# Kernel optimization log

Hardware: AMD Instinct MI355X
Metric: run time of the kernel (lower is better)

The kernel has to match this reference:

```python
import jax, jax.numpy as jnp
import numpy as np

NUM_HEADS = 8
GROUPS = 32  # min(32, 512 // 4)
EPS = 1e-5


def group_norm(y, gamma, beta):
    B, C, L = y.shape
    yg = y.reshape(B, GROUPS, -1)  # [B, G, (C//G)*L]
    mu = yg.mean(-1, keepdims=True)
    var = yg.var(-1, keepdims=True)
    yn = ((yg - mu) * jax.lax.rsqrt(var + EPS)).reshape(B, C, L)
    return yn * gamma[:, None] + beta[:, None]


def setup_inputs() -> dict:
    key = jax.random.key(0)
    ks = jax.random.split(key, 5)
    B, C, L = 4, 512, 2048
    return {
        "x": jax.random.normal(ks[0], (B, C, L), dtype=jnp.float32),
        "Wqkv": jax.random.normal(ks[1], (3 * C, C), dtype=jnp.float32) * (C ** -0.5),
        "bqkv": jax.random.normal(ks[2], (3 * C,), dtype=jnp.float32) * 0.01,
        "Wproj": jax.random.normal(ks[3], (C, C), dtype=jnp.float32) * (C ** -0.5),
        "bproj": jax.random.normal(ks[4], (C,), dtype=jnp.float32) * 0.01,
        "gamma": jnp.ones((C,), dtype=jnp.float32),
        "beta": jnp.zeros((C,), dtype=jnp.float32),
    }


def reference(x, Wqkv, bqkv, Wproj, bproj, gamma, beta):
    B, C, L = x.shape
    H = NUM_HEADS
    D = C // H
    # 1x1 Conv1d == channel-mixing matmul
    qkv = jnp.einsum('oc,bcl->bol', Wqkv, x) + bqkv[:, None]  # [B, 3C, L]
    qkv = qkv.reshape(B, 3, H, D, L)
    q, k, v = qkv[:, 0], qkv[:, 1], qkv[:, 2]
    q = jnp.clip(q, -10.0, 10.0)
    k = jnp.clip(k, -10.0, 10.0)
    v = jnp.clip(v, -10.0, 10.0)
    scale = D ** -0.5
    attn = jnp.einsum('bhdi,bhdj->bhij', q, k) * scale  # [B, H, L, L]
    attn = jnp.clip(attn, -10.0, 10.0)
    attn = jax.nn.softmax(attn, axis=-1)
    # NaN fallback: replace whole attn with identity if any NaN (matches torch branch)
    has_nan = jnp.isnan(attn).any()
    attn = jnp.where(has_nan, jnp.eye(L, dtype=x.dtype), attn)
    out = jnp.einsum('bhij,bhdj->bhdi', attn, v)  # [B, H, D, L]
    out = out.reshape(B, C, L)
    out = jnp.einsum('oc,bcl->bol', Wproj, out) + bproj[:, None]
    return group_norm(out + x, gamma, beta)
```

## Files before the change

### kernel.cpp

```cpp
#include <hip/hip_runtime.h>
#include <cstddef>

#define B_ 4
#define C_ 512
#define L_ 2048

typedef __attribute__((ext_vector_type(8))) short  short8;
typedef __attribute__((ext_vector_type(4))) float  f32x4;
typedef __attribute__((ext_vector_type(4))) unsigned short us4;

#define AS1 __attribute__((address_space(1)))
#define AS3 __attribute__((address_space(3)))

__device__ __forceinline__ float clip10(float v){ return fminf(fmaxf(v,-10.0f),10.0f); }

__device__ __forceinline__ unsigned short f2bf(float f){
  union { float f; unsigned u; } v; v.f = f;
  unsigned r = v.u + 0x7fffu + ((v.u >> 16) & 1u);
  return (unsigned short)(r >> 16);
}
__device__ __forceinline__ unsigned pk_tr(float lo, float hi){
  return __builtin_amdgcn_perm(__float_as_uint(hi), __float_as_uint(lo), 0x07060302u);
}
__device__ __forceinline__ float bf2f(unsigned short u){
  return __uint_as_float(((unsigned)u)<<16);
}
__device__ __forceinline__ void gl16(const void* g, void* l){
  __builtin_amdgcn_global_load_lds((const AS1 unsigned*)g, (AS3 unsigned*)l, 16, 0, 0);
}

__global__ __launch_bounds__(256) void prep_k(
    const float* __restrict__ x, const float* __restrict__ Wq,
    const float* __restrict__ Wp, unsigned short* __restrict__ xT,
    unsigned short* __restrict__ Wqb, unsigned short* __restrict__ Wpb)
{
  const int blk = blockIdx.x;
  const int t = threadIdx.x;
  if (blk < 4096){
    __shared__ float tile[32][33];
    const int b = blk>>10, rem = blk&1023;
    const int c0 = (rem>>6)*32, l0 = (rem&63)*32;
    const int cr = t>>3, lc = (t&7)*4;
    const float4 v = *(const float4*)(x + ((size_t)b*C_ + c0+cr)*L_ + l0 + lc);
    tile[cr][lc]=v.x; tile[cr][lc+1]=v.y; tile[cr][lc+2]=v.z; tile[cr][lc+3]=v.w;
    __syncthreads();
    const int lr = t>>3, cc = (t&7)*4;
    const us4 o = { f2bf(tile[cc][lr]), f2bf(tile[cc+1][lr]),
                    f2bf(tile[cc+2][lr]), f2bf(tile[cc+3][lr]) };
    *(us4*)(xT + ((size_t)b*L_ + l0+lr)*C_ + c0 + cc) = o;
  } else {
    const int i = (blk-4096)*256 + t;
    const int NQ = 1536*512/4;
    const float* src; unsigned short* dst; int j;
    if (i < NQ){ src = Wq; dst = Wqb; j = i; }
    else       { src = Wp; dst = Wpb; j = i - NQ; }
    const float4 v = *(const float4*)(src + (size_t)j*4);
    const us4 o = { f2bf(v.x), f2bf(v.y), f2bf(v.z), f2bf(v.w) };
    *(us4*)(dst + (size_t)j*4) = o;
  }
}

template<int MODE>
__global__ __launch_bounds__(256) void mfma_gemm(
    const unsigned short* __restrict__ Wb, const unsigned short* __restrict__ Bin,
    const float* __restrict__ bias,
    unsigned short* __restrict__ qT, unsigned short* __restrict__ kT,
    unsigned short* __restrict__ vN, float* __restrict__ yout)
{
  __shared__ unsigned short SA[128*64];
  __shared__ unsigned short SB[128*64];
  const int t = threadIdx.x;
  const int b = blockIdx.z;
  const int mb = blockIdx.y, n0 = blockIdx.x*128, m0 = mb*128;
  const int lane = t&63, w = t>>6, wm = w>>1, wn = w&1;
  const int n = lane&15, q4 = lane>>4;

  f32x4 acc[4][4];
#pragma unroll
  for (int i=0;i<4;i++)
#pragma unroll
    for (int j=0;j<4;j++) acc[i][j] = (f32x4){0.f,0.f,0.f,0.f};

  const unsigned short* Arow = Wb + (size_t)m0*512;
  const unsigned short* Brow = Bin + ((size_t)b*L_ + n0)*512;

  for (int kt=0; kt<8; kt++){
    const int k0 = kt*64;
    __syncthreads();
#pragma unroll
    for (int i=0;i<4;i++){
      const int ch = t + 256*i;
      const int row = ch>>3, lc = (ch&7) ^ (row&7);
      gl16(Arow + (size_t)row*512 + k0 + lc*8, &SA[ch*8]);
      gl16(Brow + (size_t)row*512 + k0 + lc*8, &SB[ch*8]);
    }
    __syncthreads();
#pragma unroll
    for (int kk=0;kk<2;kk++){
      short8 aF[4], bF[4];
      const int pc = ((kk*4+q4) ^ (n&7))*8;
#pragma unroll
      for (int mt=0;mt<4;mt++) aF[mt] = *(const short8*)&SA[(wm*64+mt*16+n)*64 + pc];
#pragma unroll
      for (int nt=0;nt<4;nt++) bF[nt] = *(const short8*)&SB[(wn*64+nt*16+n)*64 + pc];
#pragma unroll
      for (int mt=0;mt<4;mt++)
#pragma unroll
        for (int nt=0;nt<4;nt++)
          acc[mt][nt] = __builtin_amdgcn_mfma_f32_16x16x32_bf16(aF[mt], bF[nt], acc[mt][nt], 0,0,0);
    }
  }

  const float QS = 0.180336880f;
#pragma unroll
  for (int mt=0;mt<4;mt++){
    const int obase = m0 + wm*64 + mt*16 + q4*4;
    const float b0=bias[obase], b1=bias[obase+1], b2=bias[obase+2], b3=bias[obase+3];
#pragma unroll
    for (int nt=0;nt<4;nt++){
      const int l = n0 + wn*64 + nt*16 + n;
      float r0=acc[mt][nt][0]+b0, r1=acc[mt][nt][1]+b1,
            r2=acc[mt][nt][2]+b2, r3=acc[mt][nt][3]+b3;
      if (MODE==0){
        r0=clip10(r0); r1=clip10(r1); r2=clip10(r2); r3=clip10(r3);
        const int typ = mb>>2;
        const int oin = obase - typ*512;
        if (typ < 2){
          if (typ==0){ r0*=QS; r1*=QS; r2*=QS; r3*=QS; }
          unsigned short* dst = (typ==0) ? qT : kT;
          const us4 o = { f2bf(r0), f2bf(r1), f2bf(r2), f2bf(r3) };
          *(us4*)&dst[((size_t)b*L_ + l)*512 + oin] = o;
        } else {
          unsigned short* dst = vN + ((size_t)b*512 + oin)*L_ + l;
          dst[0]=f2bf(r0); dst[(size_t)L_]=f2bf(r1);
          dst[(size_t)2*L_]=f2bf(r2); dst[(size_t)3*L_]=f2bf(r3);
        }
      } else {
        float* dst = yout + ((size_t)b*512 + obase)*L_ + l;
        dst[0]=r0; dst[(size_t)L_]=r1; dst[(size_t)2*L_]=r2; dst[(size_t)3*L_]=r3;
      }
    }
  }
}

#define PP 72

__global__ __launch_bounds__(256,4) void attn_v8(
    const unsigned short* __restrict__ qT, const unsigned short* __restrict__ kT,
    const unsigned short* __restrict__ vN,
    unsigned short* __restrict__ Opart, float* __restrict__ den)
{
  __shared__ unsigned short s_k[64*64];
  __shared__ unsigned short s_v[64*64];
  __shared__ unsigned short s_p[128*PP];
  const int t  = threadIdx.x;
  const int io = blockIdx.x>>1, half = blockIdx.x&1;
  const int i0 = io*128;
  const int h  = blockIdx.y, b = blockIdx.z;
  const int lane = t&63, w = t>>6, n = lane&15, q4 = lane>>4;
  const int idx = ((b*8+h)*16+io)*2 + half;

  const unsigned short* kb0 = kT + (size_t)b*L_*512 + h*64;
  const unsigned short* vb  = vN + ((size_t)b*512 + h*64)*L_;

  short8 qf[2][2];
#pragma unroll
  for (int mt=0; mt<2; mt++)
#pragma unroll
    for (int kk=0; kk<2; kk++)
      qf[mt][kk] = *(const short8*)(qT + ((size_t)b*L_ + i0 + w*32 + mt*16 + n)*512
                                       + h*64 + kk*32 + q4*8);

  f32x4 oacc[2][4];
  float dacc[2];
#pragma unroll
  for (int mt=0;mt<2;mt++){ dacc[mt]=0.f;
#pragma unroll
    for (int dt=0;dt<4;dt++) oacc[mt][dt]=(f32x4){0.f,0.f,0.f,0.f}; }

  const float LIM = 14.4269504089f;
  const int jbeg = half*1024, jend = jbeg+1024;

  for (int j0=jbeg; j0<jend; j0+=64){
    __syncthreads();
#pragma unroll
    for (int i=0;i<2;i++){
      const int ch = t + 256*i, row = ch>>3, lc = (ch&7)^(row&7);
      gl16(kb0 + (size_t)(j0+row)*512 + lc*8, &s_k[ch*8]);
      gl16(vb  + (size_t)row*L_ + j0 + lc*8,  &s_v[ch*8]);
    }
    __syncthreads();

    f32x4 sacc[2][4];
#pragma unroll
    for (int mt=0;mt<2;mt++)
#pragma unroll
      for (int jt=0;jt<4;jt++) sacc[mt][jt]=(f32x4){0.f,0.f,0.f,0.f};
#pragma unroll
    for (int kk=0;kk<2;kk++){
      const int pc = ((kk*4+q4) ^ (n&7))*8;
      short8 aK[4];
#pragma unroll
      for (int jt=0;jt<4;jt++) aK[jt] = *(const short8*)&s_k[(jt*16+n)*64 + pc];
#pragma unroll
      for (int mt=0;mt<2;mt++)
#pragma unroll
        for (int jt=0;jt<4;jt++)
          sacc[mt][jt] = __builtin_amdgcn_mfma_f32_16x16x32_bf16(aK[jt], qf[mt][kk], sacc[mt][jt], 0,0,0);
    }

#pragma unroll
    for (int mt=0;mt<2;mt++)
#pragma unroll
      for (int jt=0;jt<4;jt++){
        const float e0 = __builtin_amdgcn_exp2f(__builtin_amdgcn_fmed3f(sacc[mt][jt][0],-LIM,LIM));
        const float e1 = __builtin_amdgcn_exp2f(__builtin_amdgcn_fmed3f(sacc[mt][jt][1],-LIM,LIM));
        const float e2 = __builtin_amdgcn_exp2f(__builtin_amdgcn_fmed3f(sacc[mt][jt][2],-LIM,LIM));
        const float e3 = __builtin_amdgcn_exp2f(__builtin_amdgcn_fmed3f(sacc[mt][jt][3],-LIM,LIM));
        dacc[mt] += (e0+e1)+(e2+e3);
        const unsigned long long pv =
            (unsigned long long)pk_tr(e0,e1) | ((unsigned long long)pk_tr(e2,e3)<<32);
        *(unsigned long long*)&s_p[(w*32 + mt*16 + n)*PP + jt*16 + q4*4] = pv;
      }

#pragma unroll
    for (int kk=0;kk<2;kk++){
      const int pcv = ((kk*4+q4) ^ (n&7))*8;
      short8 bV[4], pA[2];
#pragma unroll
      for (int dt=0;dt<4;dt++) bV[dt] = *(const short8*)&s_v[(dt*16+n)*64 + pcv];
#pragma unroll
      for (int mt=0;mt<2;mt++)
        pA[mt] = *(const short8*)&s_p[(w*32 + mt*16 + n)*PP + kk*32 + q4*8];
#pragma unroll
      for (int mt=0;mt<2;mt++)
#pragma unroll
        for (int dt=0;dt<4;dt++)
          oacc[mt][dt] = __builtin_amdgcn_mfma_f32_16x16x32_bf16(pA[mt], bV[kk==0?dt:dt], oacc[mt][dt], 0,0,0);
    }
  }

#pragma unroll
  for (int mt=0;mt<2;mt++){
    float d = dacc[mt];
    d += __shfl_xor(d, 16);
    d += __shfl_xor(d, 32);
    if (q4 == 0) den[(size_t)idx*128 + w*32 + mt*16 + n] = d;
  }

#pragma unroll
  for (int mt=0;mt<2;mt++)
#pragma unroll
    for (int dt=0;dt<4;dt++)
#pragma unroll
      for (int r=0;r<4;r++)
        Opart[(size_t)idx*8192 + (w*32 + mt*16 + q4*4 + r)*64 + dt*16 + n]
            = f2bf(oacc[mt][dt][r]);
}

__global__ __launch_bounds__(256) void attn_combine(
    const unsigned short* __restrict__ Opart, const float* __restrict__ den,
    unsigned short* __restrict__ attnT)
{
  __shared__ float s_inv[128];
  const int io = blockIdx.x, h = blockIdx.y, b = blockIdx.z;
  const int t = threadIdx.x;
  const int base = ((b*8+h)*16+io)*2;
  if (t < 128)
    s_inv[t] = 1.0f/(den[(size_t)base*128 + t] + den[(size_t)(base+1)*128 + t]);
  __syncthreads();
  const unsigned short* O0 = Opart + (size_t)base*8192;
  const unsigned short* O1 = O0 + 8192;
#pragma unroll
  for (int it=0; it<8; it++){
    const int chunk = it*256 + t;
    const int i = chunk>>4, c4 = (chunk&15)*4;
    const us4 a = *(const us4*)&O0[i*64 + c4];
    const us4 c = *(const us4*)&O1[i*64 + c4];
    const float inv = s_inv[i];
    const us4 o = { f2bf((bf2f(a[0])+bf2f(c[0]))*inv),
                    f2bf((bf2f(a[1])+bf2f(c[1]))*inv),
                    f2bf((bf2f(a[2])+bf2f(c[2]))*inv),
                    f2bf((bf2f(a[3])+bf2f(c[3]))*inv) };
    *(us4*)&attnT[((size_t)b*L_ + io*128 + i)*512 + h*64 + c4] = o;
  }
}

__global__ __launch_bounds__(256) void gn_stats(
    const float* __restrict__ y, const float* __restrict__ x,
    float* __restrict__ part)
{
  const int blk = blockIdx.x;
  const int b = blk>>7, g = (blk>>2)&31, s = blk&3;
  const size_t base = ((size_t)b*C_ + g*16)*L_ + s*512;
  const int t = threadIdx.x;
  float sum=0.f, sq=0.f;
#pragma unroll
  for (int i=0;i<8;i++){
    const int e = i*256 + t;
    const size_t off = base + (size_t)(e>>7)*L_ + (e&127)*4;
    const float4 vy=*(const float4*)(y+off);
    const float4 vx=*(const float4*)(x+off);
    const float a=vy.x+vx.x, c=vy.y+vx.y, d=vy.z+vx.z, f=vy.w+vx.w;
    sum += (a+c)+(d+f);
    sq  += (a*a+c*c)+(d*d+f*f);
  }
  for (int off=32;off>0;off>>=1){
    sum += __shfl_down(sum,off);
    sq  += __shfl_down(sq,off);
  }
  __shared__ float red[8];
  if ((t&63)==0){ red[(t>>6)*2]=sum; red[(t>>6)*2+1]=sq; }
  __syncthreads();
  if (t==0){
    part[blk*2+0] = red[0]+red[2]+red[4]+red[6];
    part[blk*2+1] = red[1]+red[3]+red[5]+red[7];
  }
}

__global__ __launch_bounds__(256) void gn_apply(
    const float* __restrict__ y, const float* __restrict__ x,
    const float* __restrict__ part,
    const float* __restrict__ gamma, const float* __restrict__ beta,
    float* __restrict__ out)
{
  const int blk = blockIdx.x;
  const int b = blk>>7, g = (blk>>2)&31, s = blk&3;
  const int bg8 = (blk & ~3)*2;
  const float sum = (part[bg8+0]+part[bg8+2])+(part[bg8+4]+part[bg8+6]);
  const float sq  = (part[bg8+1]+part[bg8+3])+(part[bg8+5]+part[bg8+7]);
  const float mu = sum*(1.0f/32768.0f);
  const float rs = rsqrtf(sq*(1.0f/32768.0f) - mu*mu + 1e-5f);
  const size_t base = ((size_t)b*C_ + g*16)*L_ + s*512;
  const int t = threadIdx.x;
#pragma unroll
  for (int i=0;i<8;i++){
    const int e = i*256 + t;
    const int row = e>>7;
    const size_t off = base + (size_t)row*L_ + (e&127)*4;
    const int c = g*16 + row;
    const float ga = gamma[c], be = beta[c];
    const float4 vy=*(const float4*)(y+off);
    const float4 vx=*(const float4*)(x+off);
    float4 r;
    r.x=((vy.x+vx.x)-mu)*rs*ga+be;
    r.y=((vy.y+vx.y)-mu)*rs*ga+be;
    r.z=((vy.z+vx.z)-mu)*rs*ga+be;
    r.w=((vy.w+vx.w)-mu)*rs*ga+be;
    *(float4*)(out+off)=r;
  }
}

extern "C" void kernel_launch(void* const* d_in, const int* in_sizes, int n_in,
                              void* d_out, int out_size, void* d_ws, size_t ws_size,
                              hipStream_t stream)
{
  (void)in_sizes; (void)n_in; (void)out_size; (void)ws_size;
  const float* x     = (const float*)d_in[0];
  const float* Wqkv  = (const float*)d_in[1];
  const float* bqkv  = (const float*)d_in[2];
  const float* Wproj = (const float*)d_in[3];
  const float* bproj = (const float*)d_in[4];
  const float* gamma = (const float*)d_in[5];
  const float* beta  = (const float*)d_in[6];
  float* out = (float*)d_out;
  char* ws = (char*)d_ws;

  const size_t MB = 1024*1024;
  unsigned short* qT    = (unsigned short*)(ws);
  unsigned short* kT    = (unsigned short*)(ws +  8*MB);
  unsigned short* vN    = (unsigned short*)(ws + 16*MB);
  unsigned short* attnT = (unsigned short*)(ws + 24*MB);
  unsigned short* xT    = (unsigned short*)(ws + 32*MB);
  float*          den   = (float*)        (ws + 32*MB);
  unsigned short* Wqb   = (unsigned short*)(ws + 40*MB);
  unsigned short* Wpb   = (unsigned short*)(ws + 42*MB);
  float*          y     = (float*)        (ws + 43*MB);
  unsigned short* Opart = (unsigned short*)(ws + 43*MB);
  float*          part  = (float*)        (ws + 59*MB);


  prep_k      <<<dim3(5120),   256,0,stream>>>(x, Wqkv, Wproj, xT, Wqb, Wpb);
  mfma_gemm<0><<<dim3(16,12,4),256,0,stream>>>(Wqb, xT,    bqkv , qT,kT,vN, nullptr);
  attn_v8     <<<dim3(32,8,4), 256,0,stream>>>(qT, kT, vN, Opart, den);
  attn_combine<<<dim3(16,8,4), 256,0,stream>>>(Opart, den, attnT);
  mfma_gemm<1><<<dim3(16, 4,4),256,0,stream>>>(Wpb, attnT, bproj, nullptr,nullptr,nullptr, y);
  gn_stats    <<<dim3(512),    256,0,stream>>>(y, x, part);
  gn_apply    <<<dim3(512),    256,0,stream>>>(y, x, part, gamma, beta, out);
}
```

Baseline: 190.5 us.

## Fuse residual and group-norm stats into projection GEMM, compute softmax denominator via MFMA

Adds the residual x inside the projection GEMM epilogue and accumulates per-group sum and sum-of-squares there with wave shuffles and atomics, removing the separate gn_stats pass and the extra read of x in gn_apply. The part buffer is zeroed by an extra block in prep_k. In attention, the softmax row sums are now produced by an additional MFMA against a vector of bf16 ones instead of scalar adds and shuffles. This trades VALU work for one extra MFMA per tile, sums bf16-rounded probabilities, and makes the statistics order-nondeterministic because of float atomics.

```diff
diff --git a/kernel.cpp b/kernel.cpp
--- a/kernel.cpp
+++ b/kernel.cpp
@@ -32,7 +32,8 @@
 __global__ __launch_bounds__(256) void prep_k(
     const float* __restrict__ x, const float* __restrict__ Wq,
     const float* __restrict__ Wp, unsigned short* __restrict__ xT,
-    unsigned short* __restrict__ Wqb, unsigned short* __restrict__ Wpb)
+    unsigned short* __restrict__ Wqb, unsigned short* __restrict__ Wpb,
+    float* __restrict__ part)
 {
   const int blk = blockIdx.x;
   const int t = threadIdx.x;
@@ -48,7 +49,7 @@
     const us4 o = { f2bf(tile[cc][lr]), f2bf(tile[cc+1][lr]),
                     f2bf(tile[cc+2][lr]), f2bf(tile[cc+3][lr]) };
     *(us4*)(xT + ((size_t)b*L_ + l0+lr)*C_ + c0 + cc) = o;
-  } else {
+  } else if (blk < 5120){
     const int i = (blk-4096)*256 + t;
     const int NQ = 1536*512/4;
     const float* src; unsigned short* dst; int j;
@@ -57,15 +58,18 @@
     const float4 v = *(const float4*)(src + (size_t)j*4);
     const us4 o = { f2bf(v.x), f2bf(v.y), f2bf(v.z), f2bf(v.w) };
     *(us4*)(dst + (size_t)j*4) = o;
+  } else {
+    part[t] = 0.f;
   }
 }
 
 template<int MODE>
 __global__ __launch_bounds__(256) void mfma_gemm(
     const unsigned short* __restrict__ Wb, const unsigned short* __restrict__ Bin,
-    const float* __restrict__ bias,
+    const float* __restrict__ bias, const float* __restrict__ xres,
     unsigned short* __restrict__ qT, unsigned short* __restrict__ kT,
-    unsigned short* __restrict__ vN, float* __restrict__ yout)
+    unsigned short* __restrict__ vN, float* __restrict__ yout,
+    float* __restrict__ part)
 {
   __shared__ unsigned short SA[128*64];
   __shared__ unsigned short SB[128*64];
@@ -116,6 +120,7 @@
   for (int mt=0;mt<4;mt++){
     const int obase = m0 + wm*64 + mt*16 + q4*4;
     const float b0=bias[obase], b1=bias[obase+1], b2=bias[obase+2], b3=bias[obase+3];
+    float gs=0.f, gq=0.f;
 #pragma unroll
     for (int nt=0;nt<4;nt++){
       const int l = n0 + wn*64 + nt*16 + n;
@@ -136,8 +141,25 @@
           dst[(size_t)2*L_]=f2bf(r2); dst[(size_t)3*L_]=f2bf(r3);
         }
       } else {
+        const float* xp = xres + ((size_t)b*512 + obase)*L_ + l;
+        const float y0=r0+xp[0], y1=r1+xp[(size_t)L_],
+                    y2=r2+xp[(size_t)2*L_], y3=r3+xp[(size_t)3*L_];
         float* dst = yout + ((size_t)b*512 + obase)*L_ + l;
-        dst[0]=r0; dst[(size_t)L_]=r1; dst[(size_t)2*L_]=r2; dst[(size_t)3*L_]=r3;
+        dst[0]=y0; dst[(size_t)L_]=y1; dst[(size_t)2*L_]=y2; dst[(size_t)3*L_]=y3;
+        gs += (y0+y1)+(y2+y3);
+        gq += (y0*y0+y1*y1)+(y2*y2+y3*y3);
+      }
+    }
+    if (MODE==1){
+#pragma unroll
+      for (int off=1; off<64; off<<=1){
+        gs += __shfl_xor(gs, off);
+        gq += __shfl_xor(gq, off);
+      }
+      if (lane==0){
+        const int g = mb*8 + wm*4 + mt;
+        atomicAdd(&part[(b*32+g)*2+0], gs);
+        atomicAdd(&part[(b*32+g)*2+1], gq);
       }
     }
   }
@@ -145,7 +167,7 @@
 
 #define PP 72
 
-__global__ __launch_bounds__(256,4) void attn_v8(
+__global__ __launch_bounds__(256,4) void attn_v9(
     const unsigned short* __restrict__ qT, const unsigned short* __restrict__ kT,
     const unsigned short* __restrict__ vN,
     unsigned short* __restrict__ Opart, float* __restrict__ den)
@@ -171,10 +193,14 @@
       qf[mt][kk] = *(const short8*)(qT + ((size_t)b*L_ + i0 + w*32 + mt*16 + n)*512
                                        + h*64 + kk*32 + q4*8);
 
+  short8 ones;
+#pragma unroll
+  for (int i=0;i<8;i++) ones[i] = (short)0x3F80;
+
   f32x4 oacc[2][4];
-  float dacc[2];
-#pragma unroll
-  for (int mt=0;mt<2;mt++){ dacc[mt]=0.f;
+  f32x4 oden[2];
+#pragma unroll
+  for (int mt=0;mt<2;mt++){ oden[mt]=(f32x4){0.f,0.f,0.f,0.f};
 #pragma unroll
     for (int dt=0;dt<4;dt++) oacc[mt][dt]=(f32x4){0.f,0.f,0.f,0.f}; }
 
@@ -217,7 +243,6 @@
         const float e1 = __builtin_amdgcn_exp2f(__builtin_amdgcn_fmed3f(sacc[mt][jt][1],-LIM,LIM));
         const float e2 = __builtin_amdgcn_exp2f(__builtin_amdgcn_fmed3f(sacc[mt][jt][2],-LIM,LIM));
         const float e3 = __builtin_amdgcn_exp2f(__builtin_amdgcn_fmed3f(sacc[mt][jt][3],-LIM,LIM));
-        dacc[mt] += (e0+e1)+(e2+e3);
         const unsigned long long pv =
             (unsigned long long)pk_tr(e0,e1) | ((unsigned long long)pk_tr(e2,e3)<<32);
         *(unsigned long long*)&s_p[(w*32 + mt*16 + n)*PP + jt*16 + q4*4] = pv;
@@ -233,19 +258,21 @@
       for (int mt=0;mt<2;mt++)
         pA[mt] = *(const short8*)&s_p[(w*32 + mt*16 + n)*PP + kk*32 + q4*8];
 #pragma unroll
-      for (int mt=0;mt<2;mt++)
+      for (int mt=0;mt<2;mt++){
 #pragma unroll
         for (int dt=0;dt<4;dt++)
-          oacc[mt][dt] = __builtin_amdgcn_mfma_f32_16x16x32_bf16(pA[mt], bV[kk==0?dt:dt], oacc[mt][dt], 0,0,0);
-    }
-  }
-
-#pragma unroll
-  for (int mt=0;mt<2;mt++){
-    float d = dacc[mt];
-    d += __shfl_xor(d, 16);
-    d += __shfl_xor(d, 32);
-    if (q4 == 0) den[(size_t)idx*128 + w*32 + mt*16 + n] = d;
+          oacc[mt][dt] = __builtin_amdgcn_mfma_f32_16x16x32_bf16(pA[mt], bV[dt], oacc[mt][dt], 0,0,0);
+        oden[mt] = __builtin_amdgcn_mfma_f32_16x16x32_bf16(pA[mt], ones, oden[mt], 0,0,0);
+      }
+    }
+  }
+
+  if (n == 0){
+#pragma unroll
+    for (int mt=0;mt<2;mt++)
+#pragma unroll
+      for (int r=0;r<4;r++)
+        den[(size_t)idx*128 + w*32 + mt*16 + q4*4 + r] = oden[mt][r];
   }
 
 #pragma unroll
@@ -286,49 +313,15 @@
   }
 }
 
-__global__ __launch_bounds__(256) void gn_stats(
-    const float* __restrict__ y, const float* __restrict__ x,
-    float* __restrict__ part)
+__global__ __launch_bounds__(256) void gn_apply(
+    const float* __restrict__ y, const float* __restrict__ part,
+    const float* __restrict__ gamma, const float* __restrict__ beta,
+    float* __restrict__ out)
 {
   const int blk = blockIdx.x;
   const int b = blk>>7, g = (blk>>2)&31, s = blk&3;
-  const size_t base = ((size_t)b*C_ + g*16)*L_ + s*512;
-  const int t = threadIdx.x;
-  float sum=0.f, sq=0.f;
-#pragma unroll
-  for (int i=0;i<8;i++){
-    const int e = i*256 + t;
-    const size_t off = base + (size_t)(e>>7)*L_ + (e&127)*4;
-    const float4 vy=*(const float4*)(y+off);
-    const float4 vx=*(const float4*)(x+off);
-    const float a=vy.x+vx.x, c=vy.y+vx.y, d=vy.z+vx.z, f=vy.w+vx.w;
-    sum += (a+c)+(d+f);
-    sq  += (a*a+c*c)+(d*d+f*f);
-  }
-  for (int off=32;off>0;off>>=1){
-    sum += __shfl_down(sum,off);
-    sq  += __shfl_down(sq,off);
-  }
-  __shared__ float red[8];
-  if ((t&63)==0){ red[(t>>6)*2]=sum; red[(t>>6)*2+1]=sq; }
-  __syncthreads();
-  if (t==0){
-    part[blk*2+0] = red[0]+red[2]+red[4]+red[6];
-    part[blk*2+1] = red[1]+red[3]+red[5]+red[7];
-  }
-}
-
-__global__ __launch_bounds__(256) void gn_apply(
-    const float* __restrict__ y, const float* __restrict__ x,
-    const float* __restrict__ part,
-    const float* __restrict__ gamma, const float* __restrict__ beta,
-    float* __restrict__ out)
-{
-  const int blk = blockIdx.x;
-  const int b = blk>>7, g = (blk>>2)&31, s = blk&3;
-  const int bg8 = (blk & ~3)*2;
-  const float sum = (part[bg8+0]+part[bg8+2])+(part[bg8+4]+part[bg8+6]);
-  const float sq  = (part[bg8+1]+part[bg8+3])+(part[bg8+5]+part[bg8+7]);
+  const float sum = part[(b*32+g)*2+0];
+  const float sq  = part[(b*32+g)*2+1];
   const float mu = sum*(1.0f/32768.0f);
   const float rs = rsqrtf(sq*(1.0f/32768.0f) - mu*mu + 1e-5f);
   const size_t base = ((size_t)b*C_ + g*16)*L_ + s*512;
@@ -341,12 +334,11 @@
     const int c = g*16 + row;
     const float ga = gamma[c], be = beta[c];
     const float4 vy=*(const float4*)(y+off);
-    const float4 vx=*(const float4*)(x+off);
     float4 r;
-    r.x=((vy.x+vx.x)-mu)*rs*ga+be;
-    r.y=((vy.y+vx.y)-mu)*rs*ga+be;
-    r.z=((vy.z+vx.z)-mu)*rs*ga+be;
-    r.w=((vy.w+vx.w)-mu)*rs*ga+be;
+    r.x=(vy.x-mu)*rs*ga+be;
+    r.y=(vy.y-mu)*rs*ga+be;
+    r.z=(vy.z-mu)*rs*ga+be;
+    r.w=(vy.w-mu)*rs*ga+be;
     *(float4*)(out+off)=r;
   }
 }
@@ -372,19 +364,17 @@
   unsigned short* vN    = (unsigned short*)(ws + 16*MB);
   unsigned short* attnT = (unsigned short*)(ws + 24*MB);
   unsigned short* xT    = (unsigned short*)(ws + 32*MB);
-  float*          den   = (float*)        (ws + 32*MB);
-  unsigned short* Wqb   = (unsigned short*)(ws + 40*MB);
-  unsigned short* Wpb   = (unsigned short*)(ws + 42*MB);
-  float*          y     = (float*)        (ws + 43*MB);
-  unsigned short* Opart = (unsigned short*)(ws + 43*MB);
-  float*          part  = (float*)        (ws + 59*MB);
-
-
-  prep_k      <<<dim3(5120),   256,0,stream>>>(x, Wqkv, Wproj, xT, Wqb, Wpb);
-  mfma_gemm<0><<<dim3(16,12,4),256,0,stream>>>(Wqb, xT,    bqkv , qT,kT,vN, nullptr);
-  attn_v8     <<<dim3(32,8,4), 256,0,stream>>>(qT, kT, vN, Opart, den);
+  float*          den   = (float*)        (ws + 41*MB);
+  unsigned short* Wqb   = (unsigned short*)(ws + 42*MB);
+  unsigned short* Wpb   = (unsigned short*)(ws + 44*MB);
+  float*          y     = (float*)        (ws + 45*MB);
+  unsigned short* Opart = (unsigned short*)(ws + 45*MB);
+  float*          part  = (float*)        (ws + 61*MB);
+
+  prep_k      <<<dim3(5121),   256,0,stream>>>(x, Wqkv, Wproj, xT, Wqb, Wpb, part);
+  mfma_gemm<0><<<dim3(16,12,4),256,0,stream>>>(Wqb, xT,    bqkv , nullptr, qT,kT,vN, nullptr, nullptr);
+  attn_v9     <<<dim3(32,8,4), 256,0,stream>>>(qT, kT, vN, Opart, den);
   attn_combine<<<dim3(16,8,4), 256,0,stream>>>(Opart, den, attnT);
-  mfma_gemm<1><<<dim3(16, 4,4),256,0,stream>>>(Wpb, attnT, bproj, nullptr,nullptr,nullptr, y);
-  gn_stats    <<<dim3(512),    256,0,stream>>>(y, x, part);
-  gn_apply    <<<dim3(512),    256,0,stream>>>(y, x, part, gamma, beta, out);
-}
+  mfma_gemm<1><<<dim3(16, 4,4),256,0,stream>>>(Wpb, attnT, bproj, x, nullptr,nullptr,nullptr, y, part);
+  gn_apply    <<<dim3(512),    256,0,stream>>>(y, part, gamma, beta, out);
+}
```

Measured after the change: 189.0 us. No clear change (-0.8%).
